# Optimization experiments

Hardware: AMD Instinct MI355X
Metric: run time of the kernel (lower is better)

## Reference

```python
import jax, jax.numpy as jnp
import numpy as np

N, E, G, H = 5000, 50000, 8, 4
GAT_DIMS = [(1536, 1024), (1024, 512), (512, 256)]
MLP_DIMS = [(256, 128), (128, 64), (64, 32), (32, 16), (16, 1)]
GATE_DIMS = [(256, 128), (128, 1)]
NEG_SLOPE = 0.2
EPS = 1e-16


def setup_inputs() -> dict:
    key = jax.random.key(0)
    keys = iter(jax.random.split(key, 80))

    def nrm(shape, s=0.05):
        return jax.random.normal(next(keys), shape, jnp.float32) * s

    inp = {}
    inp["x"] = jax.random.normal(next(keys), (N, 1536), jnp.float32)
    inp["edge_index"] = jax.random.randint(next(keys), (2, E), 0, N)
    inp["batch"] = jnp.sort(jax.random.randint(next(keys), (N,), 0, G))
    for i, (di, do) in enumerate(GAT_DIMS, 1):
        inp[f"Wl{i}"] = nrm((di, H * do))
        inp[f"bl{i}"] = jnp.zeros((H * do,), jnp.float32)
        inp[f"Wr{i}"] = nrm((di, H * do))
        inp[f"br{i}"] = jnp.zeros((H * do,), jnp.float32)
        inp[f"att{i}"] = nrm((H, do))
        inp[f"b{i}"] = jnp.zeros((do,), jnp.float32)
    for i, (di, do) in enumerate(MLP_DIMS):
        inp[f"Wm{i}"] = nrm((di, do))
        inp[f"bm{i}"] = jnp.zeros((do,), jnp.float32)
    for i, (di, do) in enumerate(GATE_DIMS):
        inp[f"Wg{i}"] = nrm((di, do))
        inp[f"bg{i}"] = jnp.zeros((do,), jnp.float32)
    return inp


def _gatv2(x, src, dst, Wl, bl, Wr, br, att, bias):
    # PyG GATv2Conv, concat=False: mean over heads.
    C = att.shape[1]
    xl = (x @ Wl + bl).reshape(-1, H, C)  # source-side transform [N,H,C]
    xr = (x @ Wr + br).reshape(-1, H, C)  # target-side transform [N,H,C]
    # edge scores: att . leaky_relu(x_j + x_i)  -> [E',H]
    s = jnp.sum(jax.nn.leaky_relu(xl[src] + xr[dst], negative_slope=NEG_SLOPE) * att, axis=-1)
    # segment softmax over destination node neighborhoods
    m = jax.ops.segment_max(s, dst, num_segments=N)
    ex = jnp.exp(s - m[dst])
    den = jax.ops.segment_sum(ex, dst, num_segments=N)
    alpha = ex / (den[dst] + EPS)
    out = jax.ops.segment_sum(alpha[:, :, None] * xl[src], dst, num_segments=N)  # [N,H,C]
    return out.mean(axis=1) + bias


def _forward(x, edge_index, batch, params):
    loop = jnp.arange(N)
    src = jnp.concatenate([edge_index[0], loop])  # add_self_loops=True (PyG default)
    dst = jnp.concatenate([edge_index[1], loop])
    for i in (1, 2, 3):
        x = jax.nn.relu(_gatv2(x, src, dst,
                               params[f"Wl{i}"], params[f"bl{i}"],
                               params[f"Wr{i}"], params[f"br{i}"],
                               params[f"att{i}"], params[f"b{i}"]))
    # AttentionalAggregation: segment-softmax(gate_nn(x)) weighted sum over graphs
    gate = jax.nn.relu(x @ params["Wg0"] + params["bg0"]) @ params["Wg1"] + params["bg1"]
    g = gate[:, 0]
    m = jax.ops.segment_max(g, batch, num_segments=G)
    ex = jnp.exp(g - m[batch])
    den = jax.ops.segment_sum(ex, batch, num_segments=G)
    w = ex / (den[batch] + EPS)
    h = jax.ops.segment_sum(w[:, None] * x, batch, num_segments=G)  # [G,256]
    for i in range(4):
        h = jax.nn.relu(h @ params[f"Wm{i}"] + params[f"bm{i}"])
    return h @ params["Wm4"] + params["bm4"]  # [G,1]


def reference(x, edge_index, batch,
              Wl1, bl1, Wr1, br1, att1, b1,
              Wl2, bl2, Wr2, br2, att2, b2,
              Wl3, bl3, Wr3, br3, att3, b3,
              Wm0, bm0, Wm1, bm1, Wm2, bm2, Wm3, bm3, Wm4, bm4,
              Wg0, bg0, Wg1, bg1):
    params = dict(locals())
    for k in ("x", "edge_index", "batch"):
        params.pop(k)
    return _forward(x, edge_index, batch, params)
```

## Files before the change

kernel.cpp:

```cpp
#include <hip/hip_runtime.h>
#include <math.h>

#define NN 5000
#define NNP 5120
#define NE 50000
#define NEE 55000
#define NG 8
#define NH 4

typedef __attribute__((ext_vector_type(8))) _Float16 half8;
typedef __attribute__((ext_vector_type(4))) _Float16 half4;
typedef __attribute__((ext_vector_type(4))) float floatx4;


__device__ inline float waveSum(float v) {
    #pragma unroll
    for (int o = 32; o > 0; o >>= 1) v += __shfl_xor(v, o, 64);
    return v;
}
__device__ inline float waveMax(float v) {
    #pragma unroll
    for (int o = 32; o > 0; o >>= 1) v = fmaxf(v, __shfl_xor(v, o, 64));
    return v;
}

__device__ __forceinline__ void gload_lds16(const _Float16* g, _Float16* l) {
    __builtin_amdgcn_global_load_lds(
        (__attribute__((address_space(1))) void*)g,
        (__attribute__((address_space(3))) void*)l,
        16, 0, 0);
}


__global__ void k_cvtA(const float* __restrict__ X, _Float16* __restrict__ A0, int n) {
    int i = blockIdx.x * 256 + threadIdx.x;
    if (i >= n) return;
    A0[i] = (_Float16)X[i];
}

__global__ __launch_bounds__(256) void k_cvtWT(const float* __restrict__ W,
        _Float16* __restrict__ B0, int K, int M)
{
    __shared__ float tile[32][33];
    int m0 = blockIdx.x * 32, k0 = blockIdx.y * 32;
    int tx = threadIdx.x & 31, ty = threadIdx.x >> 5;
    #pragma unroll
    for (int i = 0; i < 4; ++i)
        tile[ty + 8 * i][tx] = W[(size_t)(k0 + ty + 8 * i) * M + m0 + tx];
    __syncthreads();
    #pragma unroll
    for (int i = 0; i < 4; ++i) {
        int mm = ty + 8 * i, kk = tx;
        B0[(size_t)(m0 + mm) * K + kk + k0] = (_Float16)tile[kk][mm];
    }
}

__global__ __launch_bounds__(256) void gemm_mfma_f16(
    const _Float16* __restrict__ A0, const _Float16* __restrict__ B0,
    const float* __restrict__ bias, _Float16* __restrict__ C,
    int Mrows, int K, int N)
{
    __shared__ __align__(16) _Float16 As[2][128 * 32];
    __shared__ __align__(16) _Float16 Bs[2][128 * 32];

    const int tid = threadIdx.x;
    const int wave = tid >> 6;
    const int lane = tid & 63;
    const int wm = (wave >> 1) * 64;
    const int wn = (wave & 1) * 64;
    const int lm = lane & 15;
    const int swz = (((lane >> 4) ^ ((lane >> 1) & 3)) << 3);
    const int rowBase = blockIdx.y * 128;
    const int colBase = blockIdx.x * 128;

    floatx4 acc[4][4];
    #pragma unroll
    for (int i = 0; i < 4; ++i)
        #pragma unroll
        for (int j = 0; j < 4; ++j)
            acc[i][j] = (floatx4){0.f, 0.f, 0.f, 0.f};

    const int sr = lane >> 2;
    const int scol = (((lane & 3) ^ ((lane >> 3) & 3)) << 3);
    const _Float16* gA = A0 + (size_t)(rowBase + wave * 32 + sr) * K + scol;
    const _Float16* gB = B0 + (size_t)(colBase + wave * 32 + sr) * K + scol;
    const size_t skip16 = (size_t)16 * K;
    const int lo0 = (wave * 32) * 32;
    const int lo1 = (wave * 32 + 16) * 32;

    gload_lds16(gA, &As[0][lo0]);
    gload_lds16(gA + skip16, &As[0][lo1]);
    gload_lds16(gB, &Bs[0][lo0]);
    gload_lds16(gB + skip16, &Bs[0][lo1]);
    __syncthreads();

    const int nk = K >> 5;
    for (int t = 0; t < nk; ++t) {
        const int p = t & 1;
        if (t + 1 < nk) {
            const int k1 = (t + 1) << 5;
            gload_lds16(gA + k1, &As[p ^ 1][lo0]);
            gload_lds16(gA + skip16 + k1, &As[p ^ 1][lo1]);
            gload_lds16(gB + k1, &Bs[p ^ 1][lo0]);
            gload_lds16(gB + skip16 + k1, &Bs[p ^ 1][lo1]);
        }
        half8 a0[4], b0[4];
        #pragma unroll
        for (int i = 0; i < 4; ++i) {
            a0[i] = *(const half8*)&As[p][(wm + i * 16 + lm) * 32 + swz];
            b0[i] = *(const half8*)&Bs[p][(wn + i * 16 + lm) * 32 + swz];
        }
        #pragma unroll
        for (int i = 0; i < 4; ++i)
            #pragma unroll
            for (int j = 0; j < 4; ++j)
                acc[i][j] = __builtin_amdgcn_mfma_f32_16x16x32_f16(a0[i], b0[j], acc[i][j], 0, 0, 0);
        __syncthreads();
    }

    const int cq = (lane >> 4) * 4;
    #pragma unroll
    for (int j = 0; j < 4; ++j) {
        int col = colBase + wn + j * 16 + lm;
        float bv = bias[col];
        #pragma unroll
        for (int i = 0; i < 4; ++i) {
            #pragma unroll
            for (int r = 0; r < 4; ++r) {
                int grow = rowBase + wm + i * 16 + cq + r;
                if (grow < Mrows)
                    C[(size_t)grow * N + col] = (_Float16)(acc[i][j][r] + bv);
            }
        }
    }
}


__global__ void k_build_edges(const int* __restrict__ ei, int* __restrict__ src,
                              int* __restrict__ dst) {
    int i = blockIdx.x * 256 + threadIdx.x;
    if (i < NE) { src[i] = ei[i]; dst[i] = ei[NE + i]; }
    else if (i < NEE) { src[i] = i - NE; dst[i] = i - NE; }
}

__global__ void k_zero32(unsigned int* __restrict__ p, int n) {
    int i = blockIdx.x * 256 + threadIdx.x;
    if (i < n) p[i] = 0u;
}

__global__ void k_count(const int* __restrict__ dst, int* __restrict__ cnt) {
    int i = blockIdx.x * 256 + threadIdx.x;
    if (i < NEE) atomicAdd(&cnt[dst[i]], 1);
}

__global__ __launch_bounds__(256) void k_scan(const int* __restrict__ cnt,
                                              int* __restrict__ off, int* __restrict__ cur) {
    __shared__ int partial[256];
    __shared__ int ppre[257];
    int t = threadIdx.x;
    const int chunk = (NN + 255) / 256;
    int lo = t * chunk, hi = min(NN, (t + 1) * chunk);
    int s = 0;
    for (int i = lo; i < hi; ++i) s += cnt[i];
    partial[t] = s;
    __syncthreads();
    if (t == 0) {
        int acc = 0;
        for (int i = 0; i < 256; ++i) { ppre[i] = acc; acc += partial[i]; }
        ppre[256] = acc;
    }
    __syncthreads();
    int acc = ppre[t];
    for (int i = lo; i < hi; ++i) { off[i] = acc; cur[i] = acc; acc += cnt[i]; }
    if (t == 0) off[NN] = ppre[256];
}

__global__ void k_fill(const int* __restrict__ src, const int* __restrict__ dst,
                       int* __restrict__ cur, int* __restrict__ slist) {
    int e = blockIdx.x * 256 + threadIdx.x;
    if (e < NEE) { int p = atomicAdd(&cur[dst[e]], 1); slist[p] = src[e]; }
}

template<int C>
__global__ __launch_bounds__(256) void k_gat_fused(
    const _Float16* __restrict__ xl, const _Float16* __restrict__ xr,
    const float* __restrict__ att, const int* __restrict__ eoff,
    const int* __restrict__ slist, const float* __restrict__ bias,
    _Float16* __restrict__ out)
{
    constexpr int NQ = C / 256;
    __shared__ float red[NH * C];
    const int n = blockIdx.x;
    const int h = threadIdx.x >> 6;
    const int lane = threadIdx.x & 63;

    float4 xr_reg[NQ], att_reg[NQ], acc[NQ];
    {
        const _Float16* xrow = xr + (size_t)n * (NH * C) + h * C;
        const float* ah   = att + h * C;
        #pragma unroll
        for (int q = 0; q < NQ; ++q) {
            int off = q * 256 + lane * 4;
            half4 hv = *(const half4*)(xrow + off);
            xr_reg[q] = make_float4((float)hv[0], (float)hv[1], (float)hv[2], (float)hv[3]);
            att_reg[q] = *(const float4*)(ah + off);
            acc[q] = make_float4(0.f, 0.f, 0.f, 0.f);
        }
    }
    float m = -INFINITY, den = 0.f;
    const int start = eoff[n], end = eoff[n + 1];

    for (int j = start; j < end; ++j) {
        int s = slist[j];
        const _Float16* xlr = xl + (size_t)s * (NH * C) + h * C;
        float4 xv[NQ];
        float ps = 0.f;
        #pragma unroll
        for (int q = 0; q < NQ; ++q) {
            half4 hv = *(const half4*)(xlr + q * 256 + lane * 4);
            xv[q] = make_float4((float)hv[0], (float)hv[1], (float)hv[2], (float)hv[3]);
            float vx = xv[q].x + xr_reg[q].x;
            float vy = xv[q].y + xr_reg[q].y;
            float vz = xv[q].z + xr_reg[q].z;
            float vw = xv[q].w + xr_reg[q].w;
            vx = vx > 0.f ? vx : 0.2f * vx;
            vy = vy > 0.f ? vy : 0.2f * vy;
            vz = vz > 0.f ? vz : 0.2f * vz;
            vw = vw > 0.f ? vw : 0.2f * vw;
            ps = fmaf(vx, att_reg[q].x, ps);
            ps = fmaf(vy, att_reg[q].y, ps);
            ps = fmaf(vz, att_reg[q].z, ps);
            ps = fmaf(vw, att_reg[q].w, ps);
        }
        ps = waveSum(ps);
        float m_new = fmaxf(m, ps);
        float scale = expf(m - m_new);
        float ex = expf(ps - m_new);
        den = den * scale + ex;
        m = m_new;
        #pragma unroll
        for (int q = 0; q < NQ; ++q) {
            acc[q].x = fmaf(ex, xv[q].x, acc[q].x * scale);
            acc[q].y = fmaf(ex, xv[q].y, acc[q].y * scale);
            acc[q].z = fmaf(ex, xv[q].z, acc[q].z * scale);
            acc[q].w = fmaf(ex, xv[q].w, acc[q].w * scale);
        }
    }

    float inv = 1.f / (den + 1e-16f);
    #pragma unroll
    for (int q = 0; q < NQ; ++q) {
        int off = q * 256 + lane * 4;
        float4 r;
        r.x = acc[q].x * inv; r.y = acc[q].y * inv;
        r.z = acc[q].z * inv; r.w = acc[q].w * inv;
        *(float4*)&red[h * C + off] = r;
    }
    __syncthreads();

    int t = threadIdx.x;
    for (int c4 = t; c4 < C / 4; c4 += 256) {
        int c = c4 * 4;
        float4 r0 = *(const float4*)&red[0 * C + c];
        float4 r1 = *(const float4*)&red[1 * C + c];
        float4 r2 = *(const float4*)&red[2 * C + c];
        float4 r3 = *(const float4*)&red[3 * C + c];
        float4 bv = *(const float4*)(bias + c);
        half4 o;
        o[0] = (_Float16)fmaxf((r0.x + r1.x + r2.x + r3.x) * 0.25f + bv.x, 0.f);
        o[1] = (_Float16)fmaxf((r0.y + r1.y + r2.y + r3.y) * 0.25f + bv.y, 0.f);
        o[2] = (_Float16)fmaxf((r0.z + r1.z + r2.z + r3.z) * 0.25f + bv.z, 0.f);
        o[3] = (_Float16)fmaxf((r0.w + r1.w + r2.w + r3.w) * 0.25f + bv.w, 0.f);
        *(half4*)(out + (size_t)n * C + c) = o;
    }
}


__global__ __launch_bounds__(128) void k_gate(
    const _Float16* __restrict__ x, const float* __restrict__ Wg0,
    const float* __restrict__ bg0, const float* __restrict__ Wg1,
    const float* __restrict__ bg1, float* __restrict__ g)
{
    int n = blockIdx.x;
    int t = threadIdx.x;
    __shared__ float xs[256];
    __shared__ float wsum[2];
    const _Float16* xp = x + (size_t)n * 256;
    xs[t] = (float)xp[t]; xs[t + 128] = (float)xp[t + 128];
    __syncthreads();
    float acc = bg0[t];
    for (int k = 0; k < 256; ++k) acc = fmaf(xs[k], Wg0[k * 128 + t], acc);
    acc = acc > 0.f ? acc : 0.f;
    float prod = acc * Wg1[t];
    prod = waveSum(prod);
    if ((t & 63) == 0) wsum[t >> 6] = prod;
    __syncthreads();
    if (t == 0) g[n] = wsum[0] + wsum[1] + bg1[0];
}

__global__ void k_group_bounds(const int* __restrict__ batch, int* __restrict__ gstart,
                               int* __restrict__ gend) {
    int n = blockIdx.x * 256 + threadIdx.x;
    if (n >= NN) return;
    int b = batch[n];
    if (n == 0 || batch[n - 1] != b) gstart[b] = n;
    if (n == NN - 1 || batch[n + 1] != b) gend[b] = n + 1;
}

__global__ __launch_bounds__(256) void k_pool_stats(
    const float* __restrict__ g, const int* __restrict__ gstart,
    const int* __restrict__ gend, float* __restrict__ mOut,
    float* __restrict__ invdenOut)
{
    int gi = blockIdx.x;
    int t = threadIdx.x;
    int s0 = gstart[gi], e0 = gend[gi];
    __shared__ float red[4];
    float mx = -1e30f;
    for (int n = s0 + t; n < e0; n += 256) mx = fmaxf(mx, g[n]);
    float wm = waveMax(mx);
    if ((t & 63) == 0) red[t >> 6] = wm;
    __syncthreads();
    float m = fmaxf(fmaxf(red[0], red[1]), fmaxf(red[2], red[3]));
    __syncthreads();
    float sm = 0.f;
    for (int n = s0 + t; n < e0; n += 256) sm += expf(g[n] - m);
    sm = waveSum(sm);
    if ((t & 63) == 0) red[t >> 6] = sm;
    __syncthreads();
    if (t == 0) {
        float den = red[0] + red[1] + red[2] + red[3] + 1e-16f;
        mOut[gi] = m;
        invdenOut[gi] = 1.f / den;
    }
}

#define PCH 16
__global__ __launch_bounds__(256) void k_pool_acc(
    const _Float16* __restrict__ x, const float* __restrict__ g,
    const int* __restrict__ batch, const float* __restrict__ m,
    const float* __restrict__ invden, float* __restrict__ hpool)
{
    int base = blockIdx.x * PCH;
    int t = threadIdx.x;
    float acc = 0.f;
    int cur = -1;
    for (int i = 0; i < PCH; ++i) {
        int n = base + i;
        if (n >= NN) break;
        int b = batch[n];
        if (b != cur) {
            if (cur >= 0) atomicAdd(&hpool[cur * 256 + t], acc);
            cur = b; acc = 0.f;
        }
        float w = expf(g[n] - m[b]) * invden[b];
        acc = fmaf(w, (float)x[(size_t)n * 256 + t], acc);
    }
    if (cur >= 0) atomicAdd(&hpool[cur * 256 + t], acc);
}

__global__ __launch_bounds__(256) void k_mlp(
    const float* __restrict__ hpool,
    const float* __restrict__ Wm0, const float* __restrict__ bm0,
    const float* __restrict__ Wm1, const float* __restrict__ bm1,
    const float* __restrict__ Wm2, const float* __restrict__ bm2,
    const float* __restrict__ Wm3, const float* __restrict__ bm3,
    const float* __restrict__ Wm4, const float* __restrict__ bm4,
    float* __restrict__ out)
{
    __shared__ float bufA[8 * 256];
    __shared__ float bufB[8 * 128];
    int t = threadIdx.x;
    for (int i = t; i < 8 * 256; i += 256) bufA[i] = hpool[i];
    __syncthreads();
    for (int i = t; i < 8 * 128; i += 256) {
        int r = i >> 7, c = i & 127;
        float acc = bm0[c];
        for (int k = 0; k < 256; ++k) acc = fmaf(bufA[r * 256 + k], Wm0[k * 128 + c], acc);
        bufB[i] = fmaxf(acc, 0.f);
    }
    __syncthreads();
    for (int i = t; i < 8 * 64; i += 256) {
        int r = i >> 6, c = i & 63;
        float acc = bm1[c];
        for (int k = 0; k < 128; ++k) acc = fmaf(bufB[r * 128 + k], Wm1[k * 64 + c], acc);
        bufA[i] = fmaxf(acc, 0.f);
    }
    __syncthreads();
    for (int i = t; i < 8 * 32; i += 256) {
        int r = i >> 5, c = i & 31;
        float acc = bm2[c];
        for (int k = 0; k < 64; ++k) acc = fmaf(bufA[r * 64 + k], Wm2[k * 32 + c], acc);
        bufB[i] = fmaxf(acc, 0.f);
    }
    __syncthreads();
    for (int i = t; i < 8 * 16; i += 256) {
        int r = i >> 4, c = i & 15;
        float acc = bm3[c];
        for (int k = 0; k < 32; ++k) acc = fmaf(bufB[r * 32 + k], Wm3[k * 16 + c], acc);
        bufA[i] = fmaxf(acc, 0.f);
    }
    __syncthreads();
    if (t < 8) {
        float acc = bm4[0];
        for (int k = 0; k < 16; ++k) acc = fmaf(bufA[t * 16 + k], Wm4[k], acc);
        out[t] = acc;
    }
}


static void run_gat_layer(const _Float16* ain, int K, int C,
                          const float* Wl, const float* bl,
                          const float* Wr, const float* br,
                          const float* att, const float* bias,
                          _Float16* wb0, _Float16* xl, _Float16* xr,
                          const int* eoff, const int* slist,
                          _Float16* xout, hipStream_t stream)
{
    int HC = NH * C;
    dim3 ggrid(HC / 128, NNP / 128);
    dim3 tgrid(HC / 32, K / 32);
    k_cvtWT<<<tgrid, 256, 0, stream>>>(Wl, wb0, K, HC);
    gemm_mfma_f16<<<ggrid, 256, 0, stream>>>(ain, wb0, bl, xl, NN, K, HC);
    k_cvtWT<<<tgrid, 256, 0, stream>>>(Wr, wb0, K, HC);
    gemm_mfma_f16<<<ggrid, 256, 0, stream>>>(ain, wb0, br, xr, NN, K, HC);

    if (C == 1024)
        k_gat_fused<1024><<<NN, 256, 0, stream>>>(xl, xr, att, eoff, slist, bias, xout);
    else if (C == 512)
        k_gat_fused<512><<<NN, 256, 0, stream>>>(xl, xr, att, eoff, slist, bias, xout);
    else
        k_gat_fused<256><<<NN, 256, 0, stream>>>(xl, xr, att, eoff, slist, bias, xout);
}

extern "C" void kernel_launch(void* const* d_in, const int* in_sizes, int n_in,
                              void* d_out, int out_size, void* d_ws, size_t ws_size,
                              hipStream_t stream) {
    const float* x      = (const float*)d_in[0];
    const int* ei       = (const int*)d_in[1];
    const int* batch    = (const int*)d_in[2];
    const float* Wl1 = (const float*)d_in[3];  const float* bl1 = (const float*)d_in[4];
    const float* Wr1 = (const float*)d_in[5];  const float* br1 = (const float*)d_in[6];
    const float* att1= (const float*)d_in[7];  const float* b1  = (const float*)d_in[8];
    const float* Wl2 = (const float*)d_in[9];  const float* bl2 = (const float*)d_in[10];
    const float* Wr2 = (const float*)d_in[11]; const float* br2 = (const float*)d_in[12];
    const float* att2= (const float*)d_in[13]; const float* b2  = (const float*)d_in[14];
    const float* Wl3 = (const float*)d_in[15]; const float* bl3 = (const float*)d_in[16];
    const float* Wr3 = (const float*)d_in[17]; const float* br3 = (const float*)d_in[18];
    const float* att3= (const float*)d_in[19]; const float* b3  = (const float*)d_in[20];
    const float* Wm0 = (const float*)d_in[21]; const float* bm0 = (const float*)d_in[22];
    const float* Wm1 = (const float*)d_in[23]; const float* bm1 = (const float*)d_in[24];
    const float* Wm2 = (const float*)d_in[25]; const float* bm2 = (const float*)d_in[26];
    const float* Wm3 = (const float*)d_in[27]; const float* bm3 = (const float*)d_in[28];
    const float* Wm4 = (const float*)d_in[29]; const float* bm4 = (const float*)d_in[30];
    const float* Wg0 = (const float*)d_in[31]; const float* bg0 = (const float*)d_in[32];
    const float* Wg1 = (const float*)d_in[33]; const float* bg1 = (const float*)d_in[34];
    float* out = (float*)d_out;

    float* ws = (float*)d_ws;
    size_t o = 0;
    _Float16* xl  = (_Float16*)(ws + o); o += (size_t)NNP * 4096 / 2;
    _Float16* xr  = (_Float16*)(ws + o); o += (size_t)NNP * 4096 / 2;
    _Float16* x1  = (_Float16*)(ws + o); o += (size_t)NNP * 1024 / 2;
    _Float16* x2  = (_Float16*)(ws + o); o += (size_t)NNP * 512 / 2;
    _Float16* x3  = (_Float16*)(ws + o); o += (size_t)NNP * 256 / 2;
    _Float16* a0p = (_Float16*)(ws + o); o += (size_t)NNP * 1536 / 2;
    _Float16* wb0 = (_Float16*)(ws + o); o += (size_t)1536 * 4096 / 2;
    int* srcA    = (int*)(ws + o); o += NEE;
    int* dstA    = (int*)(ws + o); o += NEE;
    int* cnt     = (int*)(ws + o); o += NN;
    int* eoff    = (int*)(ws + o); o += NN + 1;
    int* cur     = (int*)(ws + o); o += NN;
    int* slist   = (int*)(ws + o); o += NEE;
    float* g     = ws + o; o += NN;
    int* gstart  = (int*)(ws + o); o += NG;
    int* gend    = (int*)(ws + o); o += NG;
    float* gm    = ws + o; o += NG;
    float* ginv  = ws + o; o += NG;
    float* hpool = ws + o; o += NG * 256;

    int ebB = (NEE + 255) / 256;
    k_build_edges<<<ebB, 256, 0, stream>>>(ei, srcA, dstA);
    k_zero32<<<(NN + 255) / 256, 256, 0, stream>>>((unsigned int*)cnt, NN);
    k_count<<<ebB, 256, 0, stream>>>(dstA, cnt);
    k_scan<<<1, 256, 0, stream>>>(cnt, eoff, cur);
    k_fill<<<ebB, 256, 0, stream>>>(srcA, dstA, cur, slist);

    int nA = NN * 1536;
    k_cvtA<<<(nA + 255) / 256, 256, 0, stream>>>(x, a0p, nA);

    run_gat_layer(a0p, 1536, 1024, Wl1, bl1, Wr1, br1, att1, b1,
                  wb0, xl, xr, eoff, slist, x1, stream);
    run_gat_layer(x1,  1024, 512,  Wl2, bl2, Wr2, br2, att2, b2,
                  wb0, xl, xr, eoff, slist, x2, stream);
    run_gat_layer(x2,  512,  256,  Wl3, bl3, Wr3, br3, att3, b3,
                  wb0, xl, xr, eoff, slist, x3, stream);

    k_gate<<<NN, 128, 0, stream>>>(x3, Wg0, bg0, Wg1, bg1, g);
    k_zero32<<<1, 64, 0, stream>>>((unsigned int*)gstart, 2 * NG);
    k_group_bounds<<<(NN + 255) / 256, 256, 0, stream>>>(batch, gstart, gend);
    k_pool_stats<<<NG, 256, 0, stream>>>(g, gstart, gend, gm, ginv);
    k_zero32<<<(NG * 256 + 255) / 256, 256, 0, stream>>>((unsigned int*)hpool, NG * 256);
    k_pool_acc<<<(NN + PCH - 1) / PCH, 256, 0, stream>>>(x3, g, batch, gm, ginv, hpool);
    k_mlp<<<1, 256, 0, stream>>>(hpool, Wm0, bm0, Wm1, bm1, Wm2, bm2,
                                 Wm3, bm3, Wm4, bm4, out);
}
```

Before: 772.3 us.

## Fuse left/right GAT projections into one GEMM, add tile swizzle and prefetch

Concatenates the Wl and Wr weight transposes so a single MFMA GEMM produces an interleaved [N, 2*H*C] xl|xr buffer with split bias, instead of two launches that each read A. The GEMM also remaps workgroup IDs in an XCD-aware way and stages output through LDS so stores are coalesced 16-byte writes. The GAT aggregation kernel reads from the combined buffer, uses wider per-lane chunks, and double-buffers the next neighbour row load to hide gather latency. Costs include a larger workspace, extra LDS round trips in the epilogue, and higher register pressure in the aggregation kernel.

```diff
diff --git a/kernel.cpp b/kernel.cpp
--- a/kernel.cpp
+++ b/kernel.cpp
@@ -57,11 +57,13 @@
 
 __global__ __launch_bounds__(256) void gemm_mfma_f16(
     const _Float16* __restrict__ A0, const _Float16* __restrict__ B0,
-    const float* __restrict__ bias, _Float16* __restrict__ C,
+    const float* __restrict__ biasL, const float* __restrict__ biasR,
+    int Nhalf, _Float16* __restrict__ C,
     int Mrows, int K, int N)
 {
-    __shared__ __align__(16) _Float16 As[2][128 * 32];
-    __shared__ __align__(16) _Float16 Bs[2][128 * 32];
+    __shared__ __align__(16) _Float16 smem[2 * 2 * 128 * 32];
+    _Float16* As = smem;
+    _Float16* Bs = smem + 2 * 128 * 32;
 
     const int tid = threadIdx.x;
     const int wave = tid >> 6;
@@ -70,8 +72,15 @@
     const int wn = (wave & 1) * 64;
     const int lm = lane & 15;
     const int swz = (((lane >> 4) ^ ((lane >> 1) & 3)) << 3);
-    const int rowBase = blockIdx.y * 128;
-    const int colBase = blockIdx.x * 128;
+
+    const int nwg = gridDim.x * gridDim.y;
+    const int orig = blockIdx.y * gridDim.x + blockIdx.x;
+    int swzId = orig;
+    if ((nwg & 7) == 0) swzId = (orig & 7) * (nwg >> 3) + (orig >> 3);
+    const int bx = swzId % gridDim.x;
+    const int by = swzId / gridDim.x;
+    const int rowBase = by * 128;
+    const int colBase = bx * 128;
 
     floatx4 acc[4][4];
     #pragma unroll
@@ -88,27 +97,29 @@
     const int lo0 = (wave * 32) * 32;
     const int lo1 = (wave * 32 + 16) * 32;
 
-    gload_lds16(gA, &As[0][lo0]);
-    gload_lds16(gA + skip16, &As[0][lo1]);
-    gload_lds16(gB, &Bs[0][lo0]);
-    gload_lds16(gB + skip16, &Bs[0][lo1]);
+    gload_lds16(gA, &As[lo0]);
+    gload_lds16(gA + skip16, &As[lo1]);
+    gload_lds16(gB, &Bs[lo0]);
+    gload_lds16(gB + skip16, &Bs[lo1]);
     __syncthreads();
 
     const int nk = K >> 5;
     for (int t = 0; t < nk; ++t) {
         const int p = t & 1;
+        const int po = p * 128 * 32;
         if (t + 1 < nk) {
             const int k1 = (t + 1) << 5;
-            gload_lds16(gA + k1, &As[p ^ 1][lo0]);
-            gload_lds16(gA + skip16 + k1, &As[p ^ 1][lo1]);
-            gload_lds16(gB + k1, &Bs[p ^ 1][lo0]);
-            gload_lds16(gB + skip16 + k1, &Bs[p ^ 1][lo1]);
+            const int qo = (p ^ 1) * 128 * 32;
+            gload_lds16(gA + k1, &As[qo + lo0]);
+            gload_lds16(gA + skip16 + k1, &As[qo + lo1]);
+            gload_lds16(gB + k1, &Bs[qo + lo0]);
+            gload_lds16(gB + skip16 + k1, &Bs[qo + lo1]);
         }
         half8 a0[4], b0[4];
         #pragma unroll
         for (int i = 0; i < 4; ++i) {
-            a0[i] = *(const half8*)&As[p][(wm + i * 16 + lm) * 32 + swz];
-            b0[i] = *(const half8*)&Bs[p][(wn + i * 16 + lm) * 32 + swz];
+            a0[i] = *(const half8*)&As[po + (wm + i * 16 + lm) * 32 + swz];
+            b0[i] = *(const half8*)&Bs[po + (wn + i * 16 + lm) * 32 + swz];
         }
         #pragma unroll
         for (int i = 0; i < 4; ++i)
@@ -118,19 +129,31 @@
         __syncthreads();
     }
 
+    _Float16* Ct = smem;
     const int cq = (lane >> 4) * 4;
     #pragma unroll
     for (int j = 0; j < 4; ++j) {
-        int col = colBase + wn + j * 16 + lm;
-        float bv = bias[col];
+        int col = wn + j * 16 + lm;
+        int gcol = colBase + col;
+        float bv = (gcol < Nhalf) ? biasL[gcol] : biasR[gcol - Nhalf];
         #pragma unroll
         for (int i = 0; i < 4; ++i) {
+            int row = wm + i * 16 + cq;
             #pragma unroll
-            for (int r = 0; r < 4; ++r) {
-                int grow = rowBase + wm + i * 16 + cq + r;
-                if (grow < Mrows)
-                    C[(size_t)grow * N + col] = (_Float16)(acc[i][j][r] + bv);
-            }
+            for (int r = 0; r < 4; ++r)
+                Ct[(row + r) * 128 + col] = (_Float16)(acc[i][j][r] + bv);
+        }
+    }
+    __syncthreads();
+    const int r0 = tid >> 4;
+    const int cc = (tid & 15) * 8;
+    #pragma unroll
+    for (int ps = 0; ps < 8; ++ps) {
+        int row = ps * 16 + r0;
+        int grow = rowBase + row;
+        if (grow < Mrows) {
+            half8 v = *(const half8*)&Ct[row * 128 + cc];
+            *(half8*)&C[(size_t)grow * N + colBase + cc] = v;
         }
     }
 }
@@ -183,54 +206,71 @@
 
 template<int C>
 __global__ __launch_bounds__(256) void k_gat_fused(
-    const _Float16* __restrict__ xl, const _Float16* __restrict__ xr,
-    const float* __restrict__ att, const int* __restrict__ eoff,
-    const int* __restrict__ slist, const float* __restrict__ bias,
-    _Float16* __restrict__ out)
-{
-    constexpr int NQ = C / 256;
+    const _Float16* __restrict__ xlr, const float* __restrict__ att,
+    const int* __restrict__ eoff, const int* __restrict__ slist,
+    const float* __restrict__ bias, _Float16* __restrict__ out)
+{
+    constexpr int LD = 2 * NH * C;
+    constexpr int CH = (C >= 512) ? 8 : 4;
+    constexpr int NC = C / (64 * CH);
+    constexpr int PL = NC * CH;
     __shared__ float red[NH * C];
     const int n = blockIdx.x;
     const int h = threadIdx.x >> 6;
     const int lane = threadIdx.x & 63;
 
-    float4 xr_reg[NQ], att_reg[NQ], acc[NQ];
+    float xrv[PL], attv[PL], acc[PL];
     {
-        const _Float16* xrow = xr + (size_t)n * (NH * C) + h * C;
-        const float* ah   = att + h * C;
-        #pragma unroll
-        for (int q = 0; q < NQ; ++q) {
-            int off = q * 256 + lane * 4;
-            half4 hv = *(const half4*)(xrow + off);
-            xr_reg[q] = make_float4((float)hv[0], (float)hv[1], (float)hv[2], (float)hv[3]);
-            att_reg[q] = *(const float4*)(ah + off);
-            acc[q] = make_float4(0.f, 0.f, 0.f, 0.f);
-        }
-    }
+        const _Float16* xrrow = xlr + (size_t)n * LD + NH * C + h * C + lane * CH;
+        const float* ah = att + h * C + lane * CH;
+        #pragma unroll
+        for (int c = 0; c < NC; ++c) {
+            if constexpr (CH == 8) {
+                half8 hv = *(const half8*)(xrrow + c * 64 * CH);
+                #pragma unroll
+                for (int e = 0; e < 8; ++e) xrv[c * 8 + e] = (float)hv[e];
+            } else {
+                half4 hv = *(const half4*)(xrrow + c * 64 * CH);
+                #pragma unroll
+                for (int e = 0; e < 4; ++e) xrv[c * 4 + e] = (float)hv[e];
+            }
+            #pragma unroll
+            for (int e = 0; e < CH; e += 4) {
+                float4 a4 = *(const float4*)(ah + c * 64 * CH + e);
+                attv[c * CH + e + 0] = a4.x; attv[c * CH + e + 1] = a4.y;
+                attv[c * CH + e + 2] = a4.z; attv[c * CH + e + 3] = a4.w;
+            }
+        }
+        #pragma unroll
+        for (int e = 0; e < PL; ++e) acc[e] = 0.f;
+    }
+
     float m = -INFINITY, den = 0.f;
     const int start = eoff[n], end = eoff[n + 1];
 
+    _Float16 bufA[PL], bufB[PL];
+    auto ldrow = [&](int s, _Float16* buf) {
+        const _Float16* p = xlr + (size_t)s * LD + h * C + lane * CH;
+        #pragma unroll
+        for (int c = 0; c < NC; ++c) {
+            if constexpr (CH == 8)
+                *(half8*)&buf[c * 8] = *(const half8*)(p + c * 64 * CH);
+            else
+                *(half4*)&buf[c * 4] = *(const half4*)(p + c * 64 * CH);
+        }
+    };
+
+    if (start < end) ldrow(slist[start], bufA);
     for (int j = start; j < end; ++j) {
-        int s = slist[j];
-        const _Float16* xlr = xl + (size_t)s * (NH * C) + h * C;
-        float4 xv[NQ];
+        if (j + 1 < end) ldrow(slist[j + 1], bufB);
+        float xv[PL];
         float ps = 0.f;
         #pragma unroll
-        for (int q = 0; q < NQ; ++q) {
-            half4 hv = *(const half4*)(xlr + q * 256 + lane * 4);
-            xv[q] = make_float4((float)hv[0], (float)hv[1], (float)hv[2], (float)hv[3]);
-            float vx = xv[q].x + xr_reg[q].x;
-            float vy = xv[q].y + xr_reg[q].y;
-            float vz = xv[q].z + xr_reg[q].z;
-            float vw = xv[q].w + xr_reg[q].w;
-            vx = vx > 0.f ? vx : 0.2f * vx;
-            vy = vy > 0.f ? vy : 0.2f * vy;
-            vz = vz > 0.f ? vz : 0.2f * vz;
-            vw = vw > 0.f ? vw : 0.2f * vw;
-            ps = fmaf(vx, att_reg[q].x, ps);
-            ps = fmaf(vy, att_reg[q].y, ps);
-            ps = fmaf(vz, att_reg[q].z, ps);
-            ps = fmaf(vw, att_reg[q].w, ps);
+        for (int e = 0; e < PL; ++e) {
+            xv[e] = (float)bufA[e];
+            float v = xv[e] + xrv[e];
+            v = v > 0.f ? v : 0.2f * v;
+            ps = fmaf(v, attv[e], ps);
         }
         ps = waveSum(ps);
         float m_new = fmaxf(m, ps);
@@ -239,22 +279,25 @@
         den = den * scale + ex;
         m = m_new;
         #pragma unroll
-        for (int q = 0; q < NQ; ++q) {
-            acc[q].x = fmaf(ex, xv[q].x, acc[q].x * scale);
-            acc[q].y = fmaf(ex, xv[q].y, acc[q].y * scale);
-            acc[q].z = fmaf(ex, xv[q].z, acc[q].z * scale);
-            acc[q].w = fmaf(ex, xv[q].w, acc[q].w * scale);
-        }
+        for (int e = 0; e < PL; ++e)
+            acc[e] = fmaf(ex, xv[e], acc[e] * scale);
+        #pragma unroll
+        for (int e = 0; e < PL; ++e) bufA[e] = bufB[e];
     }
 
     float inv = 1.f / (den + 1e-16f);
     #pragma unroll
-    for (int q = 0; q < NQ; ++q) {
-        int off = q * 256 + lane * 4;
-        float4 r;
-        r.x = acc[q].x * inv; r.y = acc[q].y * inv;
-        r.z = acc[q].z * inv; r.w = acc[q].w * inv;
-        *(float4*)&red[h * C + off] = r;
+    for (int c = 0; c < NC; ++c) {
+        int off = h * C + c * 64 * CH + lane * CH;
+        #pragma unroll
+        for (int e = 0; e < CH; e += 4) {
+            float4 r;
+            r.x = acc[c * CH + e + 0] * inv;
+            r.y = acc[c * CH + e + 1] * inv;
+            r.z = acc[c * CH + e + 2] * inv;
+            r.w = acc[c * CH + e + 3] * inv;
+            *(float4*)&red[off + e] = r;
+        }
     }
     __syncthreads();
 
@@ -413,24 +456,23 @@
                           const float* Wl, const float* bl,
                           const float* Wr, const float* br,
                           const float* att, const float* bias,
-                          _Float16* wb0, _Float16* xl, _Float16* xr,
+                          _Float16* wb0, _Float16* xlr,
                           const int* eoff, const int* slist,
                           _Float16* xout, hipStream_t stream)
 {
     int HC = NH * C;
-    dim3 ggrid(HC / 128, NNP / 128);
     dim3 tgrid(HC / 32, K / 32);
     k_cvtWT<<<tgrid, 256, 0, stream>>>(Wl, wb0, K, HC);
-    gemm_mfma_f16<<<ggrid, 256, 0, stream>>>(ain, wb0, bl, xl, NN, K, HC);
-    k_cvtWT<<<tgrid, 256, 0, stream>>>(Wr, wb0, K, HC);
-    gemm_mfma_f16<<<ggrid, 256, 0, stream>>>(ain, wb0, br, xr, NN, K, HC);
+    k_cvtWT<<<tgrid, 256, 0, stream>>>(Wr, wb0 + (size_t)HC * K, K, HC);
+    dim3 ggrid(2 * HC / 128, NNP / 128);
+    gemm_mfma_f16<<<ggrid, 256, 0, stream>>>(ain, wb0, bl, br, HC, xlr, NN, K, 2 * HC);
 
     if (C == 1024)
-        k_gat_fused<1024><<<NN, 256, 0, stream>>>(xl, xr, att, eoff, slist, bias, xout);
+        k_gat_fused<1024><<<NN, 256, 0, stream>>>(xlr, att, eoff, slist, bias, xout);
     else if (C == 512)
-        k_gat_fused<512><<<NN, 256, 0, stream>>>(xl, xr, att, eoff, slist, bias, xout);
+        k_gat_fused<512><<<NN, 256, 0, stream>>>(xlr, att, eoff, slist, bias, xout);
     else
-        k_gat_fused<256><<<NN, 256, 0, stream>>>(xl, xr, att, eoff, slist, bias, xout);
+        k_gat_fused<256><<<NN, 256, 0, stream>>>(xlr, att, eoff, slist, bias, xout);
 }
 
 extern "C" void kernel_launch(void* const* d_in, const int* in_sizes, int n_in,
@@ -459,13 +501,12 @@
 
     float* ws = (float*)d_ws;
     size_t o = 0;
-    _Float16* xl  = (_Float16*)(ws + o); o += (size_t)NNP * 4096 / 2;
-    _Float16* xr  = (_Float16*)(ws + o); o += (size_t)NNP * 4096 / 2;
+    _Float16* xlr = (_Float16*)(ws + o); o += (size_t)NNP * 8192 / 2;
     _Float16* x1  = (_Float16*)(ws + o); o += (size_t)NNP * 1024 / 2;
     _Float16* x2  = (_Float16*)(ws + o); o += (size_t)NNP * 512 / 2;
     _Float16* x3  = (_Float16*)(ws + o); o += (size_t)NNP * 256 / 2;
     _Float16* a0p = (_Float16*)(ws + o); o += (size_t)NNP * 1536 / 2;
-    _Float16* wb0 = (_Float16*)(ws + o); o += (size_t)1536 * 4096 / 2;
+    _Float16* wb0 = (_Float16*)(ws + o); o += (size_t)8192 * 1536 / 2;
     int* srcA    = (int*)(ws + o); o += NEE;
     int* dstA    = (int*)(ws + o); o += NEE;
     int* cnt     = (int*)(ws + o); o += NN;
@@ -490,11 +531,11 @@
     k_cvtA<<<(nA + 255) / 256, 256, 0, stream>>>(x, a0p, nA);
 
     run_gat_layer(a0p, 1536, 1024, Wl1, bl1, Wr1, br1, att1, b1,
-                  wb0, xl, xr, eoff, slist, x1, stream);
+                  wb0, xlr, eoff, slist, x1, stream);
     run_gat_layer(x1,  1024, 512,  Wl2, bl2, Wr2, br2, att2, b2,
-                  wb0, xl, xr, eoff, slist, x2, stream);
+                  wb0, xlr, eoff, slist, x2, stream);
     run_gat_layer(x2,  512,  256,  Wl3, bl3, Wr3, br3, att3, b3,
-                  wb0, xl, xr, eoff, slist, x3, stream);
+                  wb0, xlr, eoff, slist, x3, stream);
 
     k_gate<<<NN, 128, 0, stream>>>(x3, Wg0, bg0, Wg1, bg1, g);
     k_zero32<<<1, 64, 0, stream>>>((unsigned int*)gstart, 2 * NG);
```

Result: faster. 725.9 us (-6.0%).
